# Performance work log

Measured on AMD Instinct MI355X. Metric: run time of the kernel, lower is better.

The kernel has to match this reference:

```python
import jax, jax.numpy as jnp
import numpy as np

N = 50000        # total nodes (disjoint batch of graphs)
E = 800000       # total edges
F_IN = 8         # node feature dim
S = 6            # edge feature dim
H = 20           # ECC kernel-network hidden size (hidden_states)
N_OUT = 20       # ECC output channels (n_out=hidden_states)
G = 32           # GCN channels
D1 = 16          # first dense
N_GRAPHS = 512   # graphs in batch


def setup_inputs() -> dict:
    key = jax.random.key(0)
    ks = jax.random.split(key, 24)
    r = lambda k, sh, s: jax.random.normal(k, sh, dtype=jnp.float32) * s
    return {
        "x": r(ks[0], (N, F_IN), 1.0),
        "e": r(ks[1], (E, S), 1.0),
        "edge_index": jax.random.randint(ks[2], (2, E), 0, N, dtype=jnp.int32),
        "seg": jnp.sort(jax.random.randint(ks[3], (N,), 0, N_GRAPHS, dtype=jnp.int32)),
        # ECC kernel network: S -> H -> H -> F_IN*N_OUT
        "ecc_w1": r(ks[4], (S, H), 0.4), "ecc_b1": jnp.zeros((H,), jnp.float32),
        "ecc_w2": r(ks[5], (H, H), 0.2), "ecc_b2": jnp.zeros((H,), jnp.float32),
        "ecc_w3": r(ks[6], (H, F_IN * N_OUT), 0.2), "ecc_b3": jnp.zeros((F_IN * N_OUT,), jnp.float32),
        "ecc_root": r(ks[7], (F_IN, N_OUT), 0.3), "ecc_b": jnp.zeros((N_OUT,), jnp.float32),
        "gcn1_w": r(ks[8], (N_OUT, G), 0.2), "gcn1_b": jnp.zeros((G,), jnp.float32),
        "gcn2_w": r(ks[9], (G, G), 0.2), "gcn2_b": jnp.zeros((G,), jnp.float32),
        "d1_w": r(ks[10], (G, D1), 0.2), "d1_b": jnp.zeros((D1,), jnp.float32),
        "d2_w": r(ks[11], (D1, 1), 0.2), "d2_b": jnp.zeros((1,), jnp.float32),
    }


def reference(x, e, edge_index, seg,
              ecc_w1, ecc_b1, ecc_w2, ecc_b2, ecc_w3, ecc_b3, ecc_root, ecc_b,
              gcn1_w, gcn1_b, gcn2_w, gcn2_b, d1_w, d1_b, d2_w, d2_b):
    row, col = edge_index[0], edge_index[1]  # message col -> row

    # --- ECCConv: per-edge MLP produces an [F_IN, N_OUT] filter per edge ---
    h = jax.nn.relu(e @ ecc_w1 + ecc_b1)
    h = jax.nn.relu(h @ ecc_w2 + ecc_b2)
    w_edge = (h @ ecc_w3 + ecc_b3).reshape(E, F_IN, N_OUT)   # [E, F_in, F_out]
    msg = jnp.einsum('ef,efo->eo', x[col], w_edge)            # per-edge message
    agg = jax.ops.segment_sum(msg, row, num_segments=N)
    x1 = jax.nn.relu(agg + x @ ecc_root + ecc_b)              # root + bias + relu

    # --- GCN normalization from the edge list (A + I, symmetric norm) ---
    deg = jax.ops.segment_sum(jnp.ones((E,), x.dtype), row, num_segments=N) + 1.0
    dinv = jax.lax.rsqrt(deg)
    edge_norm = (dinv[row] * dinv[col])[:, None]
    self_norm = (dinv * dinv)[:, None]

    def gcn(hin, W, b):
        hw = hin @ W
        nmsg = jax.ops.segment_sum(edge_norm * hw[col], row, num_segments=N)
        return jax.nn.relu(nmsg + self_norm * hw + b)

    x2 = gcn(x1, gcn1_w, gcn1_b)
    x3 = gcn(x2, gcn2_w, gcn2_b)

    # --- GlobalSumPool over graph ids, then MLP head ---
    pooled = jax.ops.segment_sum(x3, seg, num_segments=N_GRAPHS)  # [n_graphs, G]
    out = (pooled @ d1_w + d1_b) @ d2_w + d2_b                    # [n_graphs, 1]
    return out
```

## Files before the change

kernel.cpp:

```cpp
#include <hip/hip_runtime.h>

#define S_DIM   6
#define H_DIM   20
#define F_INN   8
#define N_OUTC  20
#define G_DIM   32
#define D1_DIM  16
#define NGRAPH  512

typedef short short8 __attribute__((ext_vector_type(8)));
typedef float floatx4 __attribute__((ext_vector_type(4)));

__device__ __forceinline__ unsigned short f2bf(float f) {
    unsigned u = __float_as_uint(f);
    return (unsigned short)((u + 0x8000u) >> 16);
}
__device__ __forceinline__ float bf2f(unsigned short s) {
    return __uint_as_float(((unsigned)s) << 16);
}

__global__ __launch_bounds__(256) void prep_kernel(
    const float* __restrict__ w3, const float* __restrict__ b3,
    unsigned short* __restrict__ B3f)
{
    int idx = blockIdx.x * 256 + threadIdx.x;
    if (idx >= 6144) return;
    int jj   = idx & 7;
    int n    = (idx >> 3) & 15;
    int quad = (idx >> 7) & 3;
    int nt   = (idx >> 9) & 1;
    int s    = idx >> 10;
    int K = 32 * s + quad * 8 + jj;
    int o = n + 16 * nt;
    float v = 0.0f;
    if (o < N_OUTC) {
        if (K < 160)      v = w3[(K >> 3) * 160 + (K & 7) * N_OUTC + o];
        else if (K < 168) v = b3[(K - 160) * N_OUTC + o];
    }
    B3f[idx] = f2bf(v);
}

__global__ __launch_bounds__(256) void loc_kernel(
    const int* __restrict__ ei, int E, int* __restrict__ cnt,
    int* __restrict__ loc)
{
    int i = blockIdx.x * 256 + threadIdx.x;
    if (i >= E) return;
    loc[i] = atomicAdd(&cnt[ei[i]], 1);
}

__global__ __launch_bounds__(256) void scanA_kernel(
    const int* __restrict__ deg, int N, int* __restrict__ bsum)
{
    int i = blockIdx.x * 256 + threadIdx.x;
    int v = (i < N) ? deg[i] : 0;
#pragma unroll
    for (int d = 1; d < 64; d <<= 1) v += __shfl_down(v, d, 64);
    __shared__ int ws[4];
    int wid = threadIdx.x >> 6;
    if ((threadIdx.x & 63) == 0) ws[wid] = v;
    __syncthreads();
    if (threadIdx.x == 0) bsum[blockIdx.x] = ws[0] + ws[1] + ws[2] + ws[3];
}

__global__ __launch_bounds__(256) void scanC_kernel(
    const int* __restrict__ deg, int N, const int* __restrict__ bsum, int nbl,
    int E, int* __restrict__ rowptr, float* __restrict__ dinv)
{
    __shared__ int ws[4];
    __shared__ int sboff;
    int t = threadIdx.x;
    {
        int v = (t < nbl && t < blockIdx.x) ? bsum[t] : 0;
#pragma unroll
        for (int d = 1; d < 64; d <<= 1) v += __shfl_down(v, d, 64);
        int wid = t >> 6;
        if ((t & 63) == 0) ws[wid] = v;
        __syncthreads();
        if (t == 0) sboff = ws[0] + ws[1] + ws[2] + ws[3];
        __syncthreads();
    }

    int i = blockIdx.x * 256 + t;
    int d0 = (i < N) ? deg[i] : 0;
    int v = d0;
#pragma unroll
    for (int d = 1; d < 64; d <<= 1) {
        int u = __shfl_up(v, d, 64);
        if ((t & 63) >= d) v += u;
    }
    __shared__ int ws2[4];
    int wid = t >> 6;
    if ((t & 63) == 63) ws2[wid] = v;
    __syncthreads();
    int woff = 0;
    for (int w = 0; w < wid; ++w) woff += ws2[w];
    if (i < N) {
        rowptr[i] = sboff + woff + v - d0;
        dinv[i] = rsqrtf((float)d0 + 1.0f);
    }
    if (blockIdx.x == 0 && t == 0) rowptr[N] = E;
}

__global__ __launch_bounds__(256) void build_kernel(
    const int* __restrict__ ei, int E, const float* __restrict__ e,
    const int* __restrict__ rowptr, const int* __restrict__ loc,
    int4* __restrict__ e_sorted)
{
    int i = blockIdx.x * 256 + threadIdx.x;
    if (i >= E) return;
    int r = ei[i];
    int c = ei[E + i];
    int p = rowptr[r] + loc[i];

    const float2* ep = (const float2*)&e[(size_t)i * S_DIM];
    float2 e0 = ep[0], e1 = ep[1], e2 = ep[2];

    int4 rec;
    rec.x = c;
    rec.y = (int)f2bf(e0.x) | ((int)f2bf(e0.y) << 16);
    rec.z = (int)f2bf(e1.x) | ((int)f2bf(e1.y) << 16);
    rec.w = (int)f2bf(e2.x) | ((int)f2bf(e2.y) << 16);
    e_sorted[p] = rec;
}

__global__ __launch_bounds__(256) void ecc_mfma_kernel(
    const int4* __restrict__ e_sorted, const float* __restrict__ x,
    const int* __restrict__ rowptr, int N, int E,
    const unsigned short* __restrict__ B3f,
    const float* __restrict__ w1, const float* __restrict__ b1,
    const float* __restrict__ w2, const float* __restrict__ b2,
    float* __restrict__ agg, int* __restrict__ col_sorted)
{
    __shared__ char smem[20480];
    __shared__ int rbounds[2];
    unsigned short (*h2b)[N_OUTC] = (unsigned short (*)[N_OUTC])smem;
    unsigned short (*xb)[F_INN]   = (unsigned short (*)[F_INN])(smem + 10240);
    float* lmsg = (float*)smem;

    int t = threadIdx.x;
    int j0 = blockIdx.x * 256;
    int jend = min(j0 + 256, E);
    int j = j0 + t;

    if (t < 2) {
        int s = (t == 0) ? j0 : (jend - 1);
        int lo = 0, hi = N - 1;
        while (lo < hi) {
            int m = (lo + hi + 1) >> 1;
            if (rowptr[m] <= s) lo = m; else hi = m - 1;
        }
        rbounds[t] = lo;
    }

    if (j < E) {
        int4 rec = e_sorted[j];
        int c = rec.x;
        col_sorted[j] = c;
        float ef[S_DIM] = {
            bf2f((unsigned short)(rec.y & 0xffff)),
            bf2f((unsigned short)((unsigned)rec.y >> 16)),
            bf2f((unsigned short)(rec.z & 0xffff)),
            bf2f((unsigned short)((unsigned)rec.z >> 16)),
            bf2f((unsigned short)(rec.w & 0xffff)),
            bf2f((unsigned short)((unsigned)rec.w >> 16))
        };

        float h1[H_DIM];
#pragma unroll
        for (int jj = 0; jj < H_DIM; ++jj) {
            float a = b1[jj];
#pragma unroll
            for (int s = 0; s < S_DIM; ++s) a = fmaf(ef[s], w1[s * H_DIM + jj], a);
            h1[jj] = fmaxf(a, 0.0f);
        }

        float h2[H_DIM];
#pragma unroll
        for (int jj = 0; jj < H_DIM; ++jj) {
            float a = b2[jj];
#pragma unroll
            for (int k = 0; k < H_DIM; ++k) a = fmaf(h1[k], w2[k * H_DIM + jj], a);
            h2[jj] = fmaxf(a, 0.0f);
        }

        const float4* xp = (const float4*)&x[(size_t)c * F_INN];
        float4 xa = xp[0], xb4 = xp[1];
        float xf[F_INN] = {xa.x, xa.y, xa.z, xa.w, xb4.x, xb4.y, xb4.z, xb4.w};

#pragma unroll
        for (int o = 0; o < N_OUTC; ++o) h2b[t][o] = f2bf(h2[o]);
#pragma unroll
        for (int f = 0; f < F_INN; ++f) xb[t][f] = f2bf(xf[f]);
    } else {
#pragma unroll
        for (int o = 0; o < N_OUTC; ++o) h2b[t][o] = 0;
#pragma unroll
        for (int f = 0; f < F_INN; ++f) xb[t][f] = 0;
    }
    __syncthreads();

    int lane = t & 63;
    int quad = lane >> 4;
    int n = lane & 15;
    const short8* Bg = (const short8*)B3f;
    short8 Bf[12];
#pragma unroll
    for (int s = 0; s < 6; ++s)
#pragma unroll
        for (int nt = 0; nt < 2; ++nt)
            Bf[s * 2 + nt] = Bg[((s * 2 + nt) * 4 + quad) * 16 + n];

    int w = t >> 6;
    floatx4 acc0s[4], acc1s[4];
#pragma unroll
    for (int T = 0; T < 4; ++T) {
        int base = w * 64 + T * 16;
        int m = base + n;

        const short8 xv8 = *(const short8*)&xb[m][0];
        float xfl[F_INN];
#pragma unroll
        for (int jj = 0; jj < F_INN; ++jj) xfl[jj] = bf2f((unsigned short)xv8[jj]);

        floatx4 acc0 = {0.f, 0.f, 0.f, 0.f};
        floatx4 acc1 = {0.f, 0.f, 0.f, 0.f};
#pragma unroll
        for (int s = 0; s < 6; ++s) {
            short8 A = {0, 0, 0, 0, 0, 0, 0, 0};
            if (s < 5) {
                float h = bf2f(h2b[m][4 * s + quad]);
#pragma unroll
                for (int jj = 0; jj < F_INN; ++jj)
                    A[jj] = (short)f2bf(h * xfl[jj]);
            } else if (quad == 0) {
                A = xv8;
            }
            acc0 = __builtin_amdgcn_mfma_f32_16x16x32_bf16(A, Bf[s * 2 + 0], acc0, 0, 0, 0);
            acc1 = __builtin_amdgcn_mfma_f32_16x16x32_bf16(A, Bf[s * 2 + 1], acc1, 0, 0, 0);
        }
        acc0s[T] = acc0;
        acc1s[T] = acc1;
    }
    __syncthreads();

#pragma unroll
    for (int T = 0; T < 4; ++T) {
        int base = w * 64 + T * 16;
#pragma unroll
        for (int r = 0; r < 4; ++r) {
            int row = base + quad * 4 + r;
            lmsg[row * N_OUTC + n] = acc0s[T][r];
            if (n < 4) lmsg[row * N_OUTC + 16 + n] = acc1s[T][r];
        }
    }
    __syncthreads();

    int r0 = rbounds[0], r1 = rbounds[1];
    int work = (r1 - r0 + 1) * 5;
    for (int ww = t; ww < work; ww += 256) {
        int row = r0 + ww / 5;
        int q = ww - (ww / 5) * 5;
        int a0 = rowptr[row], a1 = rowptr[row + 1];
        int s0 = max(a0, j0), s1 = min(a1, jend);
        float4 acc = make_float4(0.f, 0.f, 0.f, 0.f);
        for (int s = s0; s < s1; ++s) {
            const float4 v = *(const float4*)&lmsg[(s - j0) * N_OUTC + q * 4];
            acc.x += v.x; acc.y += v.y; acc.z += v.z; acc.w += v.w;
        }
        float* dst = &agg[(size_t)row * N_OUTC + q * 4];
        if (a0 >= j0 && a1 <= jend) {
            *(float4*)dst = acc;
        } else {
            unsafeAtomicAdd(dst + 0, acc.x);
            unsafeAtomicAdd(dst + 1, acc.y);
            unsafeAtomicAdd(dst + 2, acc.z);
            unsafeAtomicAdd(dst + 3, acc.w);
        }
    }
}

__global__ __launch_bounds__(256) void node1_kernel(
    const float* __restrict__ agg, const float* __restrict__ x,
    const float* __restrict__ dinv, int N,
    const float* __restrict__ root, const float* __restrict__ eb,
    const float* __restrict__ g1w,
    unsigned short* __restrict__ hws1)
{
    int n = blockIdx.x * 256 + threadIdx.x;
    if (n >= N) return;

    const float4* xp = (const float4*)&x[(size_t)n * F_INN];
    float4 xa = xp[0], xb = xp[1];
    float xf[F_INN] = {xa.x, xa.y, xa.z, xa.w, xb.x, xb.y, xb.z, xb.w};

    float x1[N_OUTC];
#pragma unroll
    for (int o = 0; o < N_OUTC; ++o) {
        float a = agg[(size_t)n * N_OUTC + o] + eb[o];
#pragma unroll
        for (int f = 0; f < F_INN; ++f) a = fmaf(xf[f], root[f * N_OUTC + o], a);
        x1[o] = fmaxf(a, 0.0f);
    }

    float di = dinv[n];
#pragma unroll
    for (int q = 0; q < 4; ++q) {
        short8 o8;
#pragma unroll
        for (int u = 0; u < 8; ++u) {
            int g = q * 8 + u;
            float a = 0.0f;
#pragma unroll
            for (int o = 0; o < N_OUTC; ++o) a = fmaf(x1[o], g1w[o * G_DIM + g], a);
            o8[u] = (short)f2bf(a * di);
        }
        *(short8*)&hws1[(size_t)n * G_DIM + q * 8] = o8;
    }
}

template<bool DO_MATMUL>
__global__ __launch_bounds__(256) void gcn_gather_kernel(
    const unsigned short* __restrict__ hws, const int* __restrict__ rowptr,
    const int* __restrict__ col_sorted, const float* __restrict__ dinv, int N,
    const float* __restrict__ bias, const float* __restrict__ w2,
    unsigned short* __restrict__ outbuf)
{
    __shared__ float x2s[64][33];
    __shared__ float w2s[G_DIM * G_DIM];

    int t = threadIdx.x;
    int nl = t >> 2;
    int q = t & 3;
    int n = blockIdx.x * 64 + nl;

    if (DO_MATMUL) {
        ((float4*)w2s)[t] = ((const float4*)w2)[t];
    }

    float xo[8];
    float di = 0.0f;
    if (n < N) {
        di = dinv[n];
        int j0 = rowptr[n], j1 = rowptr[n + 1];
        short8 sv = *(const short8*)&hws[(size_t)n * G_DIM + q * 8];
        float s[8];
#pragma unroll
        for (int k = 0; k < 8; ++k) s[k] = bf2f((unsigned short)sv[k]);
        for (int j = j0; j < j1; ++j) {
            int c = col_sorted[j];
            short8 v = *(const short8*)&hws[(size_t)c * G_DIM + q * 8];
#pragma unroll
            for (int k = 0; k < 8; ++k) s[k] += bf2f((unsigned short)v[k]);
        }
#pragma unroll
        for (int k = 0; k < 8; ++k)
            xo[k] = fmaxf(fmaf(di, s[k], bias[q * 8 + k]), 0.0f);
    } else {
#pragma unroll
        for (int k = 0; k < 8; ++k) xo[k] = 0.0f;
    }

    if (DO_MATMUL) {
#pragma unroll
        for (int k = 0; k < 8; ++k) x2s[nl][q * 8 + k] = xo[k];
        __syncthreads();
        if (n < N) {
            float a[8];
#pragma unroll
            for (int k = 0; k < 8; ++k) a[k] = 0.0f;
#pragma unroll
            for (int g = 0; g < G_DIM; ++g) {
                float xv = x2s[nl][g];
#pragma unroll
                for (int k = 0; k < 8; ++k)
                    a[k] = fmaf(xv, w2s[g * G_DIM + q * 8 + k], a[k]);
            }
            short8 o8;
#pragma unroll
            for (int k = 0; k < 8; ++k) o8[k] = (short)f2bf(a[k] * di);
            *(short8*)&outbuf[(size_t)n * G_DIM + q * 8] = o8;
        }
    } else {
        if (n < N) {
            short8 o8;
#pragma unroll
            for (int k = 0; k < 8; ++k) o8[k] = (short)f2bf(xo[k]);
            *(short8*)&outbuf[(size_t)n * G_DIM + q * 8] = o8;
        }
    }
}

__global__ __launch_bounds__(256) void pool_head_kernel(
    const unsigned short* __restrict__ x3, const int* __restrict__ seg, int N,
    const float* __restrict__ d1w, const float* __restrict__ d1b,
    const float* __restrict__ d2w, const float* __restrict__ d2b,
    float* __restrict__ out)
{
    __shared__ float red[8][G_DIM];
    __shared__ float pvec[G_DIM];
    __shared__ int bounds[2];
    int g = blockIdx.x;
    int t = threadIdx.x;
    if (t < 2) {
        int target = g + t;
        int lo = 0, hi = N;
        while (lo < hi) {
            int m = (lo + hi) >> 1;
            if (seg[m] < target) lo = m + 1; else hi = m;
        }
        bounds[t] = lo;
    }
    __syncthreads();
    int n0 = bounds[0], n1 = bounds[1];
    int ch = t & (G_DIM - 1);
    int slice = t >> 5;
    float a = 0.0f;
    for (int n = n0 + slice; n < n1; n += 8)
        a += bf2f(x3[(size_t)n * G_DIM + ch]);
    red[slice][ch] = a;
    __syncthreads();
    if (slice == 0) {
        float s = red[0][ch];
#pragma unroll
        for (int k = 1; k < 8; ++k) s += red[k][ch];
        pvec[ch] = s;
    }
    __syncthreads();
    if (t < 64) {
        float acc = 0.0f;
        if (t < D1_DIM) {
            float tj = d1b[t];
#pragma unroll
            for (int gg = 0; gg < G_DIM; ++gg)
                tj = fmaf(pvec[gg], d1w[gg * D1_DIM + t], tj);
            acc = tj * d2w[t];
        }
#pragma unroll
        for (int d = 1; d < D1_DIM; d <<= 1) acc += __shfl_down(acc, d, 64);
        if (t == 0) out[g] = acc + d2b[0];
    }
}

extern "C" void kernel_launch(void* const* d_in, const int* in_sizes, int n_in,
                              void* d_out, int out_size, void* d_ws, size_t ws_size,
                              hipStream_t stream)
{
    const float* x    = (const float*)d_in[0];
    const float* e    = (const float*)d_in[1];
    const int*   ei   = (const int*)d_in[2];
    const int*   seg  = (const int*)d_in[3];
    const float* w1   = (const float*)d_in[4];
    const float* b1   = (const float*)d_in[5];
    const float* w2   = (const float*)d_in[6];
    const float* b2   = (const float*)d_in[7];
    const float* w3   = (const float*)d_in[8];
    const float* b3   = (const float*)d_in[9];
    const float* root = (const float*)d_in[10];
    const float* eb   = (const float*)d_in[11];
    const float* g1w  = (const float*)d_in[12];
    const float* g1b  = (const float*)d_in[13];
    const float* g2w  = (const float*)d_in[14];
    const float* g2b  = (const float*)d_in[15];
    const float* d1w  = (const float*)d_in[16];
    const float* d1b  = (const float*)d_in[17];
    const float* d2w  = (const float*)d_in[18];
    const float* d2b  = (const float*)d_in[19];

    const int N = in_sizes[3];
    const int E = in_sizes[1] / S_DIM;
    float* out = (float*)d_out;

    const int nbl = (N + 255) / 256;
    const int ebl = (E + 255) / 256;

    char* ws = (char*)d_ws;
    size_t off = 0;
    auto alloc = [&](size_t elems) -> char* {
        char* p = ws + off;
        off += ((elems * 4 + 15) & ~(size_t)15);
        return p;
    };
    int*   cnt        = (int*)  alloc(N);
    float* agg        = (float*)alloc((size_t)N * N_OUTC);
    size_t zero_bytes = off;
    int*   rowptr     = (int*)  alloc(N + 1);
    int*   bsum       = (int*)  alloc(nbl);
    float* dinv       = (float*)alloc(N);
    int*   loc        = (int*)  alloc(E);
    int*   col_sorted = (int*)  alloc(E);
    unsigned short* B3f = (unsigned short*)alloc(6144 / 2);
    int4*  e_sorted   = (int4*) alloc((size_t)E * 4);
    unsigned short* hws1 = (unsigned short*)alloc((size_t)N * G_DIM / 2);
    unsigned short* hws2 = (unsigned short*)alloc((size_t)N * G_DIM / 2);
    unsigned short* x3   = (unsigned short*)alloc((size_t)N * G_DIM / 2);
    (void)ws_size;

    hipMemsetAsync(d_ws, 0, zero_bytes, stream);

    prep_kernel<<<24, 256, 0, stream>>>(w3, b3, B3f);
    loc_kernel<<<ebl, 256, 0, stream>>>(ei, E, cnt, loc);
    scanA_kernel<<<nbl, 256, 0, stream>>>(cnt, N, bsum);
    scanC_kernel<<<nbl, 256, 0, stream>>>(cnt, N, bsum, nbl, E, rowptr, dinv);
    build_kernel<<<ebl, 256, 0, stream>>>(ei, E, e, rowptr, loc, e_sorted);
    ecc_mfma_kernel<<<ebl, 256, 0, stream>>>(e_sorted, x, rowptr, N, E, B3f,
                                             w1, b1, w2, b2, agg, col_sorted);
    node1_kernel<<<nbl, 256, 0, stream>>>(agg, x, dinv, N, root, eb, g1w, hws1);
    gcn_gather_kernel<true><<<(N + 63) / 64, 256, 0, stream>>>(
        hws1, rowptr, col_sorted, dinv, N, g1b, g2w, hws2);
    gcn_gather_kernel<false><<<(N + 63) / 64, 256, 0, stream>>>(
        hws2, rowptr, col_sorted, dinv, N, g2b, nullptr, x3);
    pool_head_kernel<<<NGRAPH, 256, 0, stream>>>(x3, seg, N, d1w, d1b, d2w, d2b, out);
}
```

Before: 269.7 us.

## Fuse node root+GCN1 projection into ECC kernel for block-owned rows

Rows whose edges all fall inside one ECC block now have root transform, ReLU and the first GCN matmul computed in-kernel via shared memory, writing hws1 directly. A cleanup kernel handles the remaining rows, using a binary search to skip those already done. The goal is to avoid the agg write/read round trip and most node1 work, at the cost of extra per-thread binary searches and more ECC kernel register/LDS pressure. It also unrolls the GCN gather loop by two.

```diff
diff --git a/kernel.cpp b/kernel.cpp
--- a/kernel.cpp
+++ b/kernel.cpp
@@ -7,6 +7,7 @@
 #define G_DIM   32
 #define D1_DIM  16
 #define NGRAPH  512
+#define CAP     32
 
 typedef short short8 __attribute__((ext_vector_type(8)));
 typedef float floatx4 __attribute__((ext_vector_type(4)));
@@ -130,9 +131,13 @@
     const unsigned short* __restrict__ B3f,
     const float* __restrict__ w1, const float* __restrict__ b1,
     const float* __restrict__ w2, const float* __restrict__ b2,
-    float* __restrict__ agg, int* __restrict__ col_sorted)
+    const float* __restrict__ root, const float* __restrict__ eb,
+    const float* __restrict__ g1w,
+    float* __restrict__ agg, int* __restrict__ col_sorted,
+    unsigned short* __restrict__ hws1)
 {
     __shared__ char smem[20480];
+    __shared__ float x1buf[CAP * N_OUTC];
     __shared__ int rbounds[2];
     unsigned short (*h2b)[N_OUTC] = (unsigned short (*)[N_OUTC])smem;
     unsigned short (*xb)[F_INN]   = (unsigned short (*)[F_INN])(smem + 10240);
@@ -257,38 +262,93 @@
     __syncthreads();
 
     int r0 = rbounds[0], r1 = rbounds[1];
-    int work = (r1 - r0 + 1) * 5;
+    int nrows = r1 - r0 + 1;
+    int work = nrows * 5;
     for (int ww = t; ww < work; ww += 256) {
-        int row = r0 + ww / 5;
-        int q = ww - (ww / 5) * 5;
+        int idx = ww / 5;
+        int q = ww - idx * 5;
+        int row = r0 + idx;
         int a0 = rowptr[row], a1 = rowptr[row + 1];
         int s0 = max(a0, j0), s1 = min(a1, jend);
-        float4 acc = make_float4(0.f, 0.f, 0.f, 0.f);
+        float ac0 = 0.f, ac1 = 0.f, ac2 = 0.f, ac3 = 0.f;
         for (int s = s0; s < s1; ++s) {
             const float4 v = *(const float4*)&lmsg[(s - j0) * N_OUTC + q * 4];
-            acc.x += v.x; acc.y += v.y; acc.z += v.z; acc.w += v.w;
-        }
-        float* dst = &agg[(size_t)row * N_OUTC + q * 4];
-        if (a0 >= j0 && a1 <= jend) {
-            *(float4*)dst = acc;
+            ac0 += v.x; ac1 += v.y; ac2 += v.z; ac3 += v.w;
+        }
+        bool owned = (a0 >= j0 && a1 <= jend);
+        if (owned && idx < CAP) {
+            const float4* xp = (const float4*)&x[(size_t)row * F_INN];
+            float4 xa = xp[0], xb4 = xp[1];
+            float rx[F_INN] = {xa.x, xa.y, xa.z, xa.w, xb4.x, xb4.y, xb4.z, xb4.w};
+            float av[4] = {ac0, ac1, ac2, ac3};
+#pragma unroll
+            for (int u = 0; u < 4; ++u) {
+                int oc = q * 4 + u;
+                float a = av[u] + eb[oc];
+#pragma unroll
+                for (int f = 0; f < F_INN; ++f)
+                    a = fmaf(rx[f], root[f * N_OUTC + oc], a);
+                x1buf[idx * N_OUTC + oc] = fmaxf(a, 0.0f);
+            }
         } else {
-            unsafeAtomicAdd(dst + 0, acc.x);
-            unsafeAtomicAdd(dst + 1, acc.y);
-            unsafeAtomicAdd(dst + 2, acc.z);
-            unsafeAtomicAdd(dst + 3, acc.w);
-        }
-    }
-}
-
-__global__ __launch_bounds__(256) void node1_kernel(
+            float* dst = &agg[(size_t)row * N_OUTC + q * 4];
+            if (owned) {
+                *(float4*)dst = make_float4(ac0, ac1, ac2, ac3);
+            } else {
+                unsafeAtomicAdd(dst + 0, ac0);
+                unsafeAtomicAdd(dst + 1, ac1);
+                unsafeAtomicAdd(dst + 2, ac2);
+                unsafeAtomicAdd(dst + 3, ac3);
+            }
+        }
+    }
+    __syncthreads();
+
+    int fast = min(nrows, CAP);
+    int work2 = fast * 8;
+    for (int ww = t; ww < work2; ww += 256) {
+        int idx = ww >> 3;
+        int qc = ww & 7;
+        int row = r0 + idx;
+        int a0 = rowptr[row], a1 = rowptr[row + 1];
+        if (!(a0 >= j0 && a1 <= jend)) continue;
+        float di = rsqrtf((float)(a1 - a0) + 1.0f);
+        float m0 = 0.f, m1 = 0.f, m2 = 0.f, m3 = 0.f;
+        const float* xr = &x1buf[idx * N_OUTC];
+#pragma unroll
+        for (int o = 0; o < N_OUTC; ++o) {
+            float xv = xr[o];
+            const float4 g = *(const float4*)&g1w[o * G_DIM + qc * 4];
+            m0 = fmaf(xv, g.x, m0); m1 = fmaf(xv, g.y, m1);
+            m2 = fmaf(xv, g.z, m2); m3 = fmaf(xv, g.w, m3);
+        }
+        unsigned lo32 = (unsigned)f2bf(m0 * di) | ((unsigned)f2bf(m1 * di) << 16);
+        unsigned hi32 = (unsigned)f2bf(m2 * di) | ((unsigned)f2bf(m3 * di) << 16);
+        *(uint2*)&hws1[(size_t)row * G_DIM + qc * 4] = make_uint2(lo32, hi32);
+    }
+}
+
+__global__ __launch_bounds__(256) void cleanup_kernel(
     const float* __restrict__ agg, const float* __restrict__ x,
-    const float* __restrict__ dinv, int N,
+    const int* __restrict__ rowptr, int N,
     const float* __restrict__ root, const float* __restrict__ eb,
     const float* __restrict__ g1w,
     unsigned short* __restrict__ hws1)
 {
     int n = blockIdx.x * 256 + threadIdx.x;
     if (n >= N) return;
+    int a0 = rowptr[n], a1 = rowptr[n + 1];
+    bool contained = (a1 > a0) ? ((a0 >> 8) == ((a1 - 1) >> 8))
+                               : ((a0 & 255) != 0);
+    if (contained) {
+        int target = (a0 >> 8) << 8;
+        int lo = 0, hi = N - 1;
+        while (lo < hi) {
+            int m = (lo + hi + 1) >> 1;
+            if (rowptr[m] <= target) lo = m; else hi = m - 1;
+        }
+        if (n - lo < CAP) return;
+    }
 
     const float4* xp = (const float4*)&x[(size_t)n * F_INN];
     float4 xa = xp[0], xb = xp[1];
@@ -303,7 +363,7 @@
         x1[o] = fmaxf(a, 0.0f);
     }
 
-    float di = dinv[n];
+    float di = rsqrtf((float)(a1 - a0) + 1.0f);
 #pragma unroll
     for (int q = 0; q < 4; ++q) {
         short8 o8;
@@ -347,6 +407,7 @@
         float s[8];
 #pragma unroll
         for (int k = 0; k < 8; ++k) s[k] = bf2f((unsigned short)sv[k]);
+#pragma unroll 2
         for (int j = j0; j < j1; ++j) {
             int c = col_sorted[j];
             short8 v = *(const short8*)&hws[(size_t)c * G_DIM + q * 8];
@@ -504,8 +565,9 @@
     scanC_kernel<<<nbl, 256, 0, stream>>>(cnt, N, bsum, nbl, E, rowptr, dinv);
     build_kernel<<<ebl, 256, 0, stream>>>(ei, E, e, rowptr, loc, e_sorted);
     ecc_mfma_kernel<<<ebl, 256, 0, stream>>>(e_sorted, x, rowptr, N, E, B3f,
-                                             w1, b1, w2, b2, agg, col_sorted);
-    node1_kernel<<<nbl, 256, 0, stream>>>(agg, x, dinv, N, root, eb, g1w, hws1);
+                                             w1, b1, w2, b2, root, eb, g1w,
+                                             agg, col_sorted, hws1);
+    cleanup_kernel<<<nbl, 256, 0, stream>>>(agg, x, rowptr, N, root, eb, g1w, hws1);
     gcn_gather_kernel<true><<<(N + 63) / 64, 256, 0, stream>>>(
         hws1, rowptr, col_sorted, dinv, N, g1b, g2w, hws2);
     gcn_gather_kernel<false><<<(N + 63) / 64, 256, 0, stream>>>(
```

Result: faster. 264.4 us (-2.0%).
